# Kernel optimization log

Hardware: AMD Instinct MI355X
Metric: run time of the kernel (lower is better)

## Reference

```python
import jax, jax.numpy as jnp
import numpy as np
import math

EMBED = 1024
N_HEAD = 16
T_LEN = 2048
BATCH = 2
MLP_MULT = 4
EPS = 1e-5


def setup_inputs() -> dict:
    key = jax.random.key(0)
    ks = jax.random.split(key, 12)
    d = EMBED
    h = MLP_MULT * d
    s = 0.02
    return {
        "x": jax.random.normal(ks[0], (BATCH, T_LEN, d), dtype=jnp.float32),
        "ln1_scale": jnp.ones((d,), jnp.float32),
        "ln1_shift": jnp.zeros((d,), jnp.float32),
        "w_qkv": jax.random.normal(ks[1], (d, 3 * d), jnp.float32) * s,
        "b_qkv": jnp.zeros((3 * d,), jnp.float32),
        "ln2_scale": jnp.ones((d,), jnp.float32),
        "ln2_shift": jnp.zeros((d,), jnp.float32),
        "w_fc": jax.random.normal(ks[2], (d, h), jnp.float32) * s,
        "b_fc": jnp.zeros((h,), jnp.float32),
        "w_proj": jax.random.normal(ks[3], (h, d), jnp.float32) * s,
        "b_proj": jnp.zeros((d,), jnp.float32),
    }


def _layer_norm(x, scale, shift):
    mu = jnp.mean(x, axis=-1, keepdims=True)
    var = jnp.var(x, axis=-1, keepdims=True)
    return (x - mu) * jax.lax.rsqrt(var + EPS) * scale + shift


def _attention(h, w_qkv, b_qkv):
    B, T, C = h.shape
    hd = C // N_HEAD
    qkv = h @ w_qkv + b_qkv  # [B,T,3C]
    q, k, v = jnp.split(qkv, 3, axis=-1)
    q = q.reshape(B, T, N_HEAD, hd)
    k = k.reshape(B, T, N_HEAD, hd)
    v = v.reshape(B, T, N_HEAD, hd)
    scores = jnp.einsum("bthd,bshd->bhts", q, k) * (1.0 / math.sqrt(hd))
    causal = jnp.tril(jnp.ones((T, T), dtype=bool))
    scores = jnp.where(causal[None, None], scores, -jnp.inf)
    probs = jax.nn.softmax(scores, axis=-1)
    y = jnp.einsum("bhts,bshd->bthd", probs, v)
    return y.reshape(B, T, C)


def reference(x, ln1_scale, ln1_shift, w_qkv, b_qkv, ln2_scale, ln2_shift,
              w_fc, b_fc, w_proj, b_proj):
    x = x + _attention(_layer_norm(x, ln1_scale, ln1_shift), w_qkv, b_qkv)
    h = _layer_norm(x, ln2_scale, ln2_shift)
    # note: module names it 'gelu' but it's nn.ReLU()
    h = jax.nn.relu(h @ w_fc + b_fc) @ w_proj + b_proj
    return x + h
```

## Files before the change

### kernel.cpp

```cpp
#include <hip/hip_runtime.h>
#include <hip/hip_bf16.h>


typedef __bf16  bf16x8  __attribute__((ext_vector_type(8)));
typedef __bf16  bf16x4  __attribute__((ext_vector_type(4)));
typedef float   floatx4 __attribute__((ext_vector_type(4)));

#define T_LEN 2048
#define EMB   1024
#define NH    16
#define HD    64
#define HID   4096

#define GLOBAL_LOAD_LDS16(gp, lp) \
    __builtin_amdgcn_global_load_lds( \
        (const __attribute__((address_space(1))) void*)(gp), \
        (__attribute__((address_space(3))) void*)(lp), 16, 0, 0)

__global__ void transpose_cast(const float* __restrict__ in,
                               __bf16* __restrict__ out, int R, int C) {
    __shared__ float tile[32][33];
    int bc = blockIdx.x * 32;
    int br = blockIdx.y * 32;
    int tx = threadIdx.x;
    int ty = threadIdx.y;
    for (int i = 0; i < 32; i += 8) {
        tile[ty + i][tx] = in[(size_t)(br + ty + i) * C + bc + tx];
    }
    __syncthreads();
    for (int i = 0; i < 32; i += 8) {
        int c = bc + ty + i, r = br + tx;
        out[(size_t)c * R + r] = (__bf16)tile[tx][ty + i];
    }
}

__global__ __launch_bounds__(256)
void ln_kernel(const float* __restrict__ in, const float* __restrict__ sc,
               const float* __restrict__ sh, __bf16* __restrict__ out) {
    int row = blockIdx.x;
    const float* p = in + (size_t)row * EMB;
    int tid = threadIdx.x;
    int lane = tid & 63, wave = tid >> 6;
    float v[4];
    float s = 0.f, s2 = 0.f;
    for (int j = 0; j < 4; j++) {
        v[j] = p[tid + j * 256];
        s += v[j]; s2 += v[j] * v[j];
    }
    for (int m = 1; m < 64; m <<= 1) {
        s  += __shfl_xor(s, m);
        s2 += __shfl_xor(s2, m);
    }
    __shared__ float ssum[4], ssum2[4];
    if (lane == 0) { ssum[wave] = s; ssum2[wave] = s2; }
    __syncthreads();
    float tot  = ssum[0] + ssum[1] + ssum[2] + ssum[3];
    float tot2 = ssum2[0] + ssum2[1] + ssum2[2] + ssum2[3];
    float mean = tot * (1.f / EMB);
    float var  = tot2 * (1.f / EMB) - mean * mean;
    float rstd = rsqrtf(var + 1e-5f);
    for (int j = 0; j < 4; j++) {
        int c = tid + j * 256;
        out[(size_t)row * EMB + c] = (__bf16)((v[j] - mean) * rstd * sc[c] + sh[c]);
    }
}

__global__ __launch_bounds__(256)
void gemm_bt(const __bf16* __restrict__ A, const __bf16* __restrict__ Bt,
             const float* __restrict__ bias, const float* __restrict__ res,
             float* __restrict__ outF, __bf16* __restrict__ outB,
             int M, int N, int lda, int KL, int relu, int gx, int gz) {
    __shared__ __align__(16) __bf16 sA[2][128][32];
    __shared__ __align__(16) __bf16 sB[2][128][32];
    const int BUFE = 128 * 32;
    int tid  = threadIdx.x;
    int lane = tid & 63, wave = tid >> 6;
    int quad = lane >> 4, l16 = lane & 15;

    int i  = blockIdx.x;
    int c  = i & 7, m = i >> 3;
    int bx = m % gx;
    int p  = (m / gx) * 8 + c;
    int by = p / gz;
    int bz = p - by * gz;

    int bm = by * 128, bn = bx * 128;
    size_t k0 = (size_t)bz * KL;
    int wm = (wave & 1) * 64, wn = (wave >> 1) * 64;
    floatx4 acc[4][4] = {};

    int seg = wave * 2;
    int srow = seg * 16 + (lane >> 2);
    int scol = (lane & 3) * 8;
    const __bf16* gA0 = &A[(size_t)(bm + srow) * lda + k0 + scol];
    const __bf16* gB0 = &Bt[(size_t)(bn + srow) * lda + k0 + scol];
    __bf16* lA0 = &sA[0][seg * 16][0];
    __bf16* lB0 = &sB[0][seg * 16][0];

    GLOBAL_LOAD_LDS16(gA0, lA0);
    GLOBAL_LOAD_LDS16(gA0 + (size_t)16 * lda, lA0 + 16 * 32);
    GLOBAL_LOAD_LDS16(gB0, lB0);
    GLOBAL_LOAD_LDS16(gB0 + (size_t)16 * lda, lB0 + 16 * 32);

    int cur = 0;
    for (int kk = 0; kk < KL; kk += 32) {
        __syncthreads();
        if (kk + 32 < KL) {
            int no = (cur ^ 1) * BUFE;
            GLOBAL_LOAD_LDS16(gA0 + kk + 32, lA0 + no);
            GLOBAL_LOAD_LDS16(gA0 + kk + 32 + (size_t)16 * lda,
                              lA0 + no + 16 * 32);
            GLOBAL_LOAD_LDS16(gB0 + kk + 32, lB0 + no);
            GLOBAL_LOAD_LDS16(gB0 + kk + 32 + (size_t)16 * lda,
                              lB0 + no + 16 * 32);
        }
        bf16x8 af[4], bfr[4];
        for (int ii = 0; ii < 4; ii++)
            af[ii] = *(const bf16x8*)&sA[cur][wm + ii * 16 + l16][quad * 8];
        for (int j = 0; j < 4; j++)
            bfr[j] = *(const bf16x8*)&sB[cur][wn + j * 16 + l16][quad * 8];
        for (int ii = 0; ii < 4; ii++)
            for (int j = 0; j < 4; j++)
                acc[ii][j] = __builtin_amdgcn_mfma_f32_16x16x32_bf16(
                    af[ii], bfr[j], acc[ii][j], 0, 0, 0);
        cur ^= 1;
    }

    if (bias) {
        for (int ii = 0; ii < 4; ii++) {
            int row0 = bm + wm + ii * 16 + quad * 4;
            for (int j = 0; j < 4; j++) {
                int col = bn + wn + j * 16 + l16;
                float bv = bias[col];
                for (int r = 0; r < 4; r++) {
                    size_t idx = (size_t)(row0 + r) * N + col;
                    float cc = acc[ii][j][r] + bv;
                    if (relu) cc = fmaxf(cc, 0.f);
                    if (res)  cc += res[idx];
                    if (outF) outF[idx] = cc;
                    if (outB) outB[idx] = (__bf16)cc;
                }
            }
        }
    } else {
        __bf16* po = outB + (size_t)bz * M * N;
        for (int ii = 0; ii < 4; ii++) {
            int row0 = bm + wm + ii * 16 + quad * 4;
            for (int j = 0; j < 4; j++) {
                int col = bn + wn + j * 16 + l16;
                for (int r = 0; r < 4; r++)
                    po[(size_t)(row0 + r) * N + col] = (__bf16)acc[ii][j][r];
            }
        }
    }
}

__global__ __launch_bounds__(256)
void reduce_proj(const __bf16* __restrict__ pbuf, const float* __restrict__ x2,
                 const float* __restrict__ bias, float* __restrict__ out) {
    const size_t MN = (size_t)4096 * 1024;
    size_t i = (size_t)blockIdx.x * 256 + threadIdx.x;
    float4 r = ((const float4*)x2)[i];
    float4 bb = ((const float4*)bias)[i & 255];
    float acc0 = r.x + bb.x, acc1 = r.y + bb.y;
    float acc2 = r.z + bb.z, acc3 = r.w + bb.w;
    for (int k = 0; k < 4; k++) {
        bf16x4 pv = *(const bf16x4*)&pbuf[k * MN + i * 4];
        acc0 += (float)pv[0]; acc1 += (float)pv[1];
        acc2 += (float)pv[2]; acc3 += (float)pv[3];
    }
    float4 o = {acc0, acc1, acc2, acc3};
    ((float4*)out)[i] = o;
}

__global__ __launch_bounds__(256)
void gemm_bt_n64(const __bf16* __restrict__ A, const __bf16* __restrict__ Bt,
                 const float* __restrict__ bias, const float* __restrict__ res,
                 float* __restrict__ outF, __bf16* __restrict__ outB,
                 int M, int N, int K, int relu) {
    __shared__ __align__(16) __bf16 sA[128][40];
    __shared__ __align__(16) __bf16 sB[64][40];
    int tid  = threadIdx.x;
    int lane = tid & 63, wave = tid >> 6;
    int quad = lane >> 4, l16 = lane & 15;
    int bm = blockIdx.y * 128, bn = blockIdx.x * 64;
    int wm = (wave & 1) * 64, wn = (wave >> 1) * 32;
    floatx4 acc[4][2] = {};

    int srow = tid >> 2;
    int scol = (tid & 3) * 8;
    const __bf16* gA = &A[(size_t)(bm + srow) * K + scol];
    const __bf16* gB = &Bt[(size_t)(bn + srow) * K + scol];

    uint4 ra0 = *(const uint4*)gA;
    uint4 ra1 = *(const uint4*)(gA + (size_t)64 * K);
    uint4 rb0 = *(const uint4*)gB;

    for (int kk = 0; kk < K; kk += 32) {
        __syncthreads();
        *(uint4*)&sA[srow][scol]      = ra0;
        *(uint4*)&sA[srow + 64][scol] = ra1;
        *(uint4*)&sB[srow][scol]      = rb0;
        __syncthreads();
        {
            int kn = (kk + 32 < K) ? kk + 32 : kk;
            ra0 = *(const uint4*)(gA + kn);
            ra1 = *(const uint4*)(gA + kn + (size_t)64 * K);
            rb0 = *(const uint4*)(gB + kn);
        }
        bf16x8 af[4], bfr[2];
        for (int i = 0; i < 4; i++)
            af[i] = *(const bf16x8*)&sA[wm + i * 16 + l16][quad * 8];
        for (int j = 0; j < 2; j++)
            bfr[j] = *(const bf16x8*)&sB[wn + j * 16 + l16][quad * 8];
        for (int i = 0; i < 4; i++)
            for (int j = 0; j < 2; j++)
                acc[i][j] = __builtin_amdgcn_mfma_f32_16x16x32_bf16(
                    af[i], bfr[j], acc[i][j], 0, 0, 0);
    }

    for (int i = 0; i < 4; i++) {
        int row0 = bm + wm + i * 16 + quad * 4;
        for (int j = 0; j < 2; j++) {
            int col = bn + wn + j * 16 + l16;
            float bv = bias[col];
            for (int r = 0; r < 4; r++) {
                size_t idx = (size_t)(row0 + r) * N + col;
                float c = acc[i][j][r] + bv;
                if (relu) c = fmaxf(c, 0.f);
                if (res)  c += res[idx];
                if (outF) outF[idx] = c;
                if (outB) outB[idx] = (__bf16)c;
            }
        }
    }
}

__global__ __launch_bounds__(256)
void attn_kernel(const __bf16* __restrict__ qkv, const float* __restrict__ x,
                 float* __restrict__ x2) {
    __shared__ __align__(16) __bf16 sK[64][72];
    __shared__ __align__(16) __bf16 sVt[64][72];
    __shared__ __align__(16) __bf16 sP[4][16][72];
    const int tid  = threadIdx.x;
    const int lane = tid & 63, wave = tid >> 6;
    const int quad = lane >> 4, l16 = lane & 15;

    int i = blockIdx.x;
    int c = i & 7, m = i >> 3;
    const int xpair = m % 16;
    const int bh = (m / 16) * 8 + c;
    const int h  = bh & (NH - 1);
    const int b  = bh >> 4;
    const size_t rowbase = (size_t)b * T_LEN;

    const float kQScale = 0.125f * 1.44269504088896f;
    bf16x8 ones;
    for (int j = 0; j < 8; j++) ones[j] = (__bf16)1.0f;

    const int key0 = tid >> 3, m8 = tid & 7;
    const int key1 = key0 + 32;
    const __bf16* kp0 = qkv + (rowbase + key0) * 3072 + h * HD + m8 * 8 + 1024;
    const __bf16* kp1 = qkv + (rowbase + key1) * 3072 + h * HD + m8 * 8 + 1024;
    const int pc0 = ((key0 >> 3) ^ m8) * 8 + (key0 & 7);
    const int pc1 = ((key1 >> 3) ^ m8) * 8 + (key1 & 7);

    for (int ph = 0; ph < 2; ph++) {
        const int qb = ph ? (31 - xpair) : xpair;
        const int qrow = qb * 64 + wave * 16;

        bf16x8 qf[2];
        for (int ks = 0; ks < 2; ks++) {
            bf16x8 raw = *(const bf16x8*)&qkv[(rowbase + qrow + l16) * 3072
                                              + h * HD + ks * 32 + quad * 8];
            for (int j = 0; j < 8; j++)
                qf[ks][j] = (__bf16)((float)raw[j] * kQScale);
        }

        floatx4 o[4] = {}, ol = {};
        float mrow[4];
        for (int r = 0; r < 4; r++) mrow[r] = -1e30f;

        uint4 kr0 = *(const uint4*)kp0;
        uint4 kr1 = *(const uint4*)kp1;
        uint4 vr0 = *(const uint4*)(kp0 + 1024);
        uint4 vr1 = *(const uint4*)(kp1 + 1024);

        const int ntiles = qb + 1;
        for (int kt = 0; kt < ntiles; kt++) {
            __syncthreads();
            *(uint4*)&sK[key0][m8 * 8] = kr0;
            *(uint4*)&sK[key1][m8 * 8] = kr1;
            {
                bf16x8 v0 = *(bf16x8*)&vr0, v1 = *(bf16x8*)&vr1;
                for (int j = 0; j < 8; j++) sVt[m8 * 8 + j][pc0] = v0[j];
                for (int j = 0; j < 8; j++) sVt[m8 * 8 + j][pc1] = v1[j];
            }
            __syncthreads();

            {
                size_t offn = (size_t)((kt + 1 < ntiles) ? kt + 1 : kt)
                              * (64 * 3072);
                kr0 = *(const uint4*)(kp0 + offn);
                kr1 = *(const uint4*)(kp1 + offn);
                vr0 = *(const uint4*)(kp0 + offn + 1024);
                vr1 = *(const uint4*)(kp1 + offn + 1024);
            }

            floatx4 s_acc[4] = {};
            for (int jt = 0; jt < 4; jt++)
                for (int ks = 0; ks < 2; ks++) {
                    bf16x8 kf = *(const bf16x8*)&sK[jt * 16 + l16]
                                                  [ks * 32 + quad * 8];
                    s_acc[jt] = __builtin_amdgcn_mfma_f32_16x16x32_bf16(
                        qf[ks], kf, s_acc[jt], 0, 0, 0);
                }

            const int tq0 = qrow + quad * 4;
            const int k0 = kt * 64;
            float rmax[4] = {-1e30f, -1e30f, -1e30f, -1e30f};
            if (kt == qb) {
                for (int jt = 0; jt < 4; jt++) {
                    int key = k0 + jt * 16 + l16;
                    for (int r = 0; r < 4; r++) {
                        float sv = (key <= tq0 + r) ? s_acc[jt][r] : -1e30f;
                        s_acc[jt][r] = sv;
                        rmax[r] = fmaxf(rmax[r], sv);
                    }
                }
            } else {
                for (int jt = 0; jt < 4; jt++)
                    for (int r = 0; r < 4; r++)
                        rmax[r] = fmaxf(rmax[r], s_acc[jt][r]);
            }

            bool changed = false;
            float mnew[4];
            for (int r = 0; r < 4; r++) {
                float mm = rmax[r];
                mm = fmaxf(mm, __shfl_xor(mm, 1));
                mm = fmaxf(mm, __shfl_xor(mm, 2));
                mm = fmaxf(mm, __shfl_xor(mm, 4));
                mm = fmaxf(mm, __shfl_xor(mm, 8));
                mnew[r] = fmaxf(mrow[r], mm);
                changed |= (mnew[r] > mrow[r]);
            }
            if (__any(changed)) {
                for (int r = 0; r < 4; r++) {
                    float alpha = __builtin_amdgcn_exp2f(mrow[r] - mnew[r]);
                    mrow[r] = mnew[r];
                    ol[r] *= alpha;
                    for (int jt = 0; jt < 4; jt++) o[jt][r] *= alpha;
                }
            }

            for (int jt = 0; jt < 4; jt++)
                for (int r = 0; r < 4; r++) {
                    float pv = __builtin_amdgcn_exp2f(s_acc[jt][r] - mrow[r]);
                    sP[wave][quad * 4 + r][jt * 16 + l16] = (__bf16)pv;
                }

            for (int kp = 0; kp < 2; kp++) {
                bf16x8 pf = *(const bf16x8*)&sP[wave][l16][kp * 32 + quad * 8];
                ol = __builtin_amdgcn_mfma_f32_16x16x32_bf16(pf, ones, ol,
                                                             0, 0, 0);
                for (int jt2 = 0; jt2 < 4; jt2++) {
                    int d = jt2 * 16 + l16;
                    int pg = (kp * 4 + quad) ^ (d >> 3);
                    bf16x8 vf = *(const bf16x8*)&sVt[d][pg * 8];
                    o[jt2] = __builtin_amdgcn_mfma_f32_16x16x32_bf16(
                        pf, vf, o[jt2], 0, 0, 0);
                }
            }
        }

        float inv[4];
        for (int r = 0; r < 4; r++) inv[r] = __builtin_amdgcn_rcpf(ol[r]);
        for (int jt2 = 0; jt2 < 4; jt2++) {
            for (int r = 0; r < 4; r++) {
                int tq  = qrow + quad * 4 + r;
                int col = h * HD + jt2 * 16 + l16;
                size_t gi = (rowbase + tq) * EMB + col;
                x2[gi] = x[gi] + o[jt2][r] * inv[r];
            }
        }
    }
}

extern "C" void kernel_launch(void* const* d_in, const int* in_sizes, int n_in,
                              void* d_out, int out_size, void* d_ws, size_t ws_size,
                              hipStream_t stream) {
    const float* x      = (const float*)d_in[0];
    const float* ln1_s  = (const float*)d_in[1];
    const float* ln1_b  = (const float*)d_in[2];
    const float* w_qkv  = (const float*)d_in[3];
    const float* b_qkv  = (const float*)d_in[4];
    const float* ln2_s  = (const float*)d_in[5];
    const float* ln2_b  = (const float*)d_in[6];
    const float* w_fc   = (const float*)d_in[7];
    const float* b_fc   = (const float*)d_in[8];
    const float* w_proj = (const float*)d_in[9];
    const float* b_proj = (const float*)d_in[10];
    float* out = (float*)d_out;

    const int M = 2 * T_LEN;
    char* ws = (char*)d_ws;
    size_t off = 0;
    auto alloc = [&](size_t bytes) {
        void* p = ws + off; off += (bytes + 255) & ~(size_t)255; return p;
    };
    __bf16* wpj_t  = (__bf16*)alloc((size_t)1024 * 4096 * 2);
    float*  x2     = (float*) alloc((size_t)M * 1024 * 4);
    __bf16* hfc    = (__bf16*)alloc((size_t)M * 4096 * 2);
    size_t mark = off;
    __bf16* wqkv_t = (__bf16*)alloc((size_t)3072 * 1024 * 2);
    __bf16* wfc_t  = (__bf16*)alloc((size_t)4096 * 1024 * 2);
    __bf16* h1     = (__bf16*)alloc((size_t)M * 1024 * 2);
    __bf16* h2     = (__bf16*)alloc((size_t)M * 1024 * 2);
    __bf16* qkvb   = (__bf16*)alloc((size_t)M * 3072 * 2);
    __bf16* pbuf = (__bf16*)(ws + mark);
    size_t need = mark + (size_t)4 * M * 1024 * 2;
    bool can_split = ws_size >= need;

    dim3 tb(32, 8);
    transpose_cast<<<dim3(3072 / 32, 1024 / 32), tb, 0, stream>>>(w_qkv, wqkv_t, 1024, 3072);
    transpose_cast<<<dim3(4096 / 32, 1024 / 32), tb, 0, stream>>>(w_fc,  wfc_t,  1024, 4096);
    transpose_cast<<<dim3(1024 / 32, 4096 / 32), tb, 0, stream>>>(w_proj, wpj_t, 4096, 1024);

    ln_kernel<<<M, 256, 0, stream>>>(x, ln1_s, ln1_b, h1);

    gemm_bt<<<24 * 32, 256, 0, stream>>>(
        h1, wqkv_t, b_qkv, nullptr, nullptr, qkvb, M, 3072, 1024, 1024, 0,
        24, 1);

    attn_kernel<<<512, 256, 0, stream>>>(qkvb, x, x2);

    ln_kernel<<<M, 256, 0, stream>>>(x2, ln2_s, ln2_b, h2);

    gemm_bt<<<32 * 32, 256, 0, stream>>>(
        h2, wfc_t, b_fc, nullptr, nullptr, hfc, M, 4096, 1024, 1024, 1,
        32, 1);

    if (can_split) {
        gemm_bt<<<8 * 32 * 4, 256, 0, stream>>>(
            hfc, wpj_t, nullptr, nullptr, nullptr, pbuf, M, 1024, 4096, 1024, 0,
            8, 4);
        reduce_proj<<<(M * 1024 / 4) / 256, 256, 0, stream>>>(
            pbuf, x2, b_proj, out);
    } else {
        gemm_bt_n64<<<dim3(1024 / 64, M / 128), 256, 0, stream>>>(
            hfc, wpj_t, b_proj, x2, out, nullptr, M, 1024, 4096, 0);
    }
}
```

Measured before the change: 343.0 us.

## Double-buffer K/V tiles in attention and assign one query block per workgroup

The attention kernel now holds two LDS buffers for K and transposed V. The next tile is written to shared memory while the current tile is computed, which leaves one barrier per iteration instead of two. The paired-query-block scheme, where one block handled a short and a long causal row for load balance, is dropped. Instead 1024 blocks each take one query block, with the longest blocks scheduled first. This trades the explicit balancing for more parallelism and LDS double buffering, at the cost of doubled K/V LDS use.

```diff
diff --git a/kernel.cpp b/kernel.cpp
--- a/kernel.cpp
+++ b/kernel.cpp
@@ -239,8 +239,8 @@
 __global__ __launch_bounds__(256)
 void attn_kernel(const __bf16* __restrict__ qkv, const float* __restrict__ x,
                  float* __restrict__ x2) {
-    __shared__ __align__(16) __bf16 sK[64][72];
-    __shared__ __align__(16) __bf16 sVt[64][72];
+    __shared__ __align__(16) __bf16 sK[2][64][72];
+    __shared__ __align__(16) __bf16 sVt[2][64][72];
     __shared__ __align__(16) __bf16 sP[4][16][72];
     const int tid  = threadIdx.x;
     const int lane = tid & 63, wave = tid >> 6;
@@ -248,11 +248,12 @@
 
     int i = blockIdx.x;
     int c = i & 7, m = i >> 3;
-    const int xpair = m % 16;
-    const int bh = (m / 16) * 8 + c;
+    const int bh = (m & 3) * 8 + c;
+    const int qb = 31 - (m >> 2);
     const int h  = bh & (NH - 1);
     const int b  = bh >> 4;
     const size_t rowbase = (size_t)b * T_LEN;
+    const int qrow = qb * 64 + wave * 16;
 
     const float kQScale = 0.125f * 1.44269504088896f;
     bf16x8 ones;
@@ -265,124 +266,131 @@
     const int pc0 = ((key0 >> 3) ^ m8) * 8 + (key0 & 7);
     const int pc1 = ((key1 >> 3) ^ m8) * 8 + (key1 & 7);
 
-    for (int ph = 0; ph < 2; ph++) {
-        const int qb = ph ? (31 - xpair) : xpair;
-        const int qrow = qb * 64 + wave * 16;
-
-        bf16x8 qf[2];
-        for (int ks = 0; ks < 2; ks++) {
-            bf16x8 raw = *(const bf16x8*)&qkv[(rowbase + qrow + l16) * 3072
-                                              + h * HD + ks * 32 + quad * 8];
-            for (int j = 0; j < 8; j++)
-                qf[ks][j] = (__bf16)((float)raw[j] * kQScale);
-        }
-
-        floatx4 o[4] = {}, ol = {};
-        float mrow[4];
-        for (int r = 0; r < 4; r++) mrow[r] = -1e30f;
-
-        uint4 kr0 = *(const uint4*)kp0;
-        uint4 kr1 = *(const uint4*)kp1;
-        uint4 vr0 = *(const uint4*)(kp0 + 1024);
-        uint4 vr1 = *(const uint4*)(kp1 + 1024);
-
-        const int ntiles = qb + 1;
-        for (int kt = 0; kt < ntiles; kt++) {
-            __syncthreads();
-            *(uint4*)&sK[key0][m8 * 8] = kr0;
-            *(uint4*)&sK[key1][m8 * 8] = kr1;
-            {
-                bf16x8 v0 = *(bf16x8*)&vr0, v1 = *(bf16x8*)&vr1;
-                for (int j = 0; j < 8; j++) sVt[m8 * 8 + j][pc0] = v0[j];
-                for (int j = 0; j < 8; j++) sVt[m8 * 8 + j][pc1] = v1[j];
-            }
-            __syncthreads();
-
-            {
-                size_t offn = (size_t)((kt + 1 < ntiles) ? kt + 1 : kt)
-                              * (64 * 3072);
-                kr0 = *(const uint4*)(kp0 + offn);
-                kr1 = *(const uint4*)(kp1 + offn);
-                vr0 = *(const uint4*)(kp0 + offn + 1024);
-                vr1 = *(const uint4*)(kp1 + offn + 1024);
-            }
-
-            floatx4 s_acc[4] = {};
+    bf16x8 qf[2];
+    for (int ks = 0; ks < 2; ks++) {
+        bf16x8 raw = *(const bf16x8*)&qkv[(rowbase + qrow + l16) * 3072
+                                          + h * HD + ks * 32 + quad * 8];
+        for (int j = 0; j < 8; j++)
+            qf[ks][j] = (__bf16)((float)raw[j] * kQScale);
+    }
+
+    floatx4 o[4] = {}, ol = {};
+    float mrow[4];
+    for (int r = 0; r < 4; r++) mrow[r] = -1e30f;
+
+    const int ntiles = qb + 1;
+    const size_t TSTEP = (size_t)64 * 3072;
+
+    uint4 kr0 = *(const uint4*)kp0;
+    uint4 kr1 = *(const uint4*)kp1;
+    uint4 vr0 = *(const uint4*)(kp0 + 1024);
+    uint4 vr1 = *(const uint4*)(kp1 + 1024);
+    {
+        *(uint4*)&sK[0][key0][m8 * 8] = kr0;
+        *(uint4*)&sK[0][key1][m8 * 8] = kr1;
+        bf16x8 v0 = *(bf16x8*)&vr0, v1 = *(bf16x8*)&vr1;
+        for (int j = 0; j < 8; j++) sVt[0][m8 * 8 + j][pc0] = v0[j];
+        for (int j = 0; j < 8; j++) sVt[0][m8 * 8 + j][pc1] = v1[j];
+    }
+    {
+        size_t o1 = (ntiles > 1) ? TSTEP : 0;
+        kr0 = *(const uint4*)(kp0 + o1);
+        kr1 = *(const uint4*)(kp1 + o1);
+        vr0 = *(const uint4*)(kp0 + o1 + 1024);
+        vr1 = *(const uint4*)(kp1 + o1 + 1024);
+    }
+    __syncthreads();
+
+    for (int kt = 0; kt < ntiles; kt++) {
+        const int cur = kt & 1, nxt = cur ^ 1;
+        if (kt + 1 < ntiles) {
+            *(uint4*)&sK[nxt][key0][m8 * 8] = kr0;
+            *(uint4*)&sK[nxt][key1][m8 * 8] = kr1;
+            bf16x8 v0 = *(bf16x8*)&vr0, v1 = *(bf16x8*)&vr1;
+            for (int j = 0; j < 8; j++) sVt[nxt][m8 * 8 + j][pc0] = v0[j];
+            for (int j = 0; j < 8; j++) sVt[nxt][m8 * 8 + j][pc1] = v1[j];
+            size_t offn = (size_t)((kt + 2 < ntiles) ? kt + 2 : kt + 1) * TSTEP;
+            kr0 = *(const uint4*)(kp0 + offn);
+            kr1 = *(const uint4*)(kp1 + offn);
+            vr0 = *(const uint4*)(kp0 + offn + 1024);
+            vr1 = *(const uint4*)(kp1 + offn + 1024);
+        }
+
+        floatx4 s_acc[4] = {};
+        for (int jt = 0; jt < 4; jt++)
+            for (int ks = 0; ks < 2; ks++) {
+                bf16x8 kf = *(const bf16x8*)&sK[cur][jt * 16 + l16]
+                                              [ks * 32 + quad * 8];
+                s_acc[jt] = __builtin_amdgcn_mfma_f32_16x16x32_bf16(
+                    qf[ks], kf, s_acc[jt], 0, 0, 0);
+            }
+
+        const int tq0 = qrow + quad * 4;
+        const int k0 = kt * 64;
+        float rmax[4] = {-1e30f, -1e30f, -1e30f, -1e30f};
+        if (kt == qb) {
+            for (int jt = 0; jt < 4; jt++) {
+                int key = k0 + jt * 16 + l16;
+                for (int r = 0; r < 4; r++) {
+                    float sv = (key <= tq0 + r) ? s_acc[jt][r] : -1e30f;
+                    s_acc[jt][r] = sv;
+                    rmax[r] = fmaxf(rmax[r], sv);
+                }
+            }
+        } else {
             for (int jt = 0; jt < 4; jt++)
-                for (int ks = 0; ks < 2; ks++) {
-                    bf16x8 kf = *(const bf16x8*)&sK[jt * 16 + l16]
-                                                  [ks * 32 + quad * 8];
-                    s_acc[jt] = __builtin_amdgcn_mfma_f32_16x16x32_bf16(
-                        qf[ks], kf, s_acc[jt], 0, 0, 0);
-                }
-
-            const int tq0 = qrow + quad * 4;
-            const int k0 = kt * 64;
-            float rmax[4] = {-1e30f, -1e30f, -1e30f, -1e30f};
-            if (kt == qb) {
-                for (int jt = 0; jt < 4; jt++) {
-                    int key = k0 + jt * 16 + l16;
-                    for (int r = 0; r < 4; r++) {
-                        float sv = (key <= tq0 + r) ? s_acc[jt][r] : -1e30f;
-                        s_acc[jt][r] = sv;
-                        rmax[r] = fmaxf(rmax[r], sv);
-                    }
-                }
-            } else {
-                for (int jt = 0; jt < 4; jt++)
-                    for (int r = 0; r < 4; r++)
-                        rmax[r] = fmaxf(rmax[r], s_acc[jt][r]);
-            }
-
-            bool changed = false;
-            float mnew[4];
+                for (int r = 0; r < 4; r++)
+                    rmax[r] = fmaxf(rmax[r], s_acc[jt][r]);
+        }
+
+        bool changed = false;
+        float mnew[4];
+        for (int r = 0; r < 4; r++) {
+            float mm = rmax[r];
+            mm = fmaxf(mm, __shfl_xor(mm, 1));
+            mm = fmaxf(mm, __shfl_xor(mm, 2));
+            mm = fmaxf(mm, __shfl_xor(mm, 4));
+            mm = fmaxf(mm, __shfl_xor(mm, 8));
+            mnew[r] = fmaxf(mrow[r], mm);
+            changed |= (mnew[r] > mrow[r]);
+        }
+        if (__any(changed)) {
             for (int r = 0; r < 4; r++) {
-                float mm = rmax[r];
-                mm = fmaxf(mm, __shfl_xor(mm, 1));
-                mm = fmaxf(mm, __shfl_xor(mm, 2));
-                mm = fmaxf(mm, __shfl_xor(mm, 4));
-                mm = fmaxf(mm, __shfl_xor(mm, 8));
-                mnew[r] = fmaxf(mrow[r], mm);
-                changed |= (mnew[r] > mrow[r]);
-            }
-            if (__any(changed)) {
-                for (int r = 0; r < 4; r++) {
-                    float alpha = __builtin_amdgcn_exp2f(mrow[r] - mnew[r]);
-                    mrow[r] = mnew[r];
-                    ol[r] *= alpha;
-                    for (int jt = 0; jt < 4; jt++) o[jt][r] *= alpha;
-                }
-            }
-
-            for (int jt = 0; jt < 4; jt++)
-                for (int r = 0; r < 4; r++) {
-                    float pv = __builtin_amdgcn_exp2f(s_acc[jt][r] - mrow[r]);
-                    sP[wave][quad * 4 + r][jt * 16 + l16] = (__bf16)pv;
-                }
-
-            for (int kp = 0; kp < 2; kp++) {
-                bf16x8 pf = *(const bf16x8*)&sP[wave][l16][kp * 32 + quad * 8];
-                ol = __builtin_amdgcn_mfma_f32_16x16x32_bf16(pf, ones, ol,
-                                                             0, 0, 0);
-                for (int jt2 = 0; jt2 < 4; jt2++) {
-                    int d = jt2 * 16 + l16;
-                    int pg = (kp * 4 + quad) ^ (d >> 3);
-                    bf16x8 vf = *(const bf16x8*)&sVt[d][pg * 8];
-                    o[jt2] = __builtin_amdgcn_mfma_f32_16x16x32_bf16(
-                        pf, vf, o[jt2], 0, 0, 0);
-                }
-            }
-        }
-
-        float inv[4];
-        for (int r = 0; r < 4; r++) inv[r] = __builtin_amdgcn_rcpf(ol[r]);
-        for (int jt2 = 0; jt2 < 4; jt2++) {
+                float alpha = __builtin_amdgcn_exp2f(mrow[r] - mnew[r]);
+                mrow[r] = mnew[r];
+                ol[r] *= alpha;
+                for (int jt = 0; jt < 4; jt++) o[jt][r] *= alpha;
+            }
+        }
+
+        for (int jt = 0; jt < 4; jt++)
             for (int r = 0; r < 4; r++) {
-                int tq  = qrow + quad * 4 + r;
-                int col = h * HD + jt2 * 16 + l16;
-                size_t gi = (rowbase + tq) * EMB + col;
-                x2[gi] = x[gi] + o[jt2][r] * inv[r];
-            }
+                float pv = __builtin_amdgcn_exp2f(s_acc[jt][r] - mrow[r]);
+                sP[wave][quad * 4 + r][jt * 16 + l16] = (__bf16)pv;
+            }
+
+        for (int kp = 0; kp < 2; kp++) {
+            bf16x8 pf = *(const bf16x8*)&sP[wave][l16][kp * 32 + quad * 8];
+            ol = __builtin_amdgcn_mfma_f32_16x16x32_bf16(pf, ones, ol, 0, 0, 0);
+            for (int jt2 = 0; jt2 < 4; jt2++) {
+                int d = jt2 * 16 + l16;
+                int pg = (kp * 4 + quad) ^ (d >> 3);
+                bf16x8 vf = *(const bf16x8*)&sVt[cur][d][pg * 8];
+                o[jt2] = __builtin_amdgcn_mfma_f32_16x16x32_bf16(
+                    pf, vf, o[jt2], 0, 0, 0);
+            }
+        }
+        __syncthreads();
+    }
+
+    float inv[4];
+    for (int r = 0; r < 4; r++) inv[r] = __builtin_amdgcn_rcpf(ol[r]);
+    for (int jt2 = 0; jt2 < 4; jt2++) {
+        for (int r = 0; r < 4; r++) {
+            int tq  = qrow + quad * 4 + r;
+            int col = h * HD + jt2 * 16 + l16;
+            size_t gi = (rowbase + tq) * EMB + col;
+            x2[gi] = x[gi] + o[jt2][r] * inv[r];
         }
     }
 }
@@ -433,7 +441,7 @@
         h1, wqkv_t, b_qkv, nullptr, nullptr, qkvb, M, 3072, 1024, 1024, 0,
         24, 1);
 
-    attn_kernel<<<512, 256, 0, stream>>>(qkvb, x, x2);
+    attn_kernel<<<1024, 256, 0, stream>>>(qkvb, x, x2);
 
     ln_kernel<<<M, 256, 0, stream>>>(x2, ln2_s, ln2_b, h2);
 
```

Result: faster. 334.8 us (-2.4%).
